# Performance work log

Hardware: AMD Instinct MI355X
Metric: run time of the kernel (lower is better)

The kernel has to match this reference:

```python
import jax, jax.numpy as jnp
import numpy as np

N = 50000   # nodes
E = 800000  # edges (before self-loops)
D = 256     # hidden_dim
H = 8       # heads
C = D // H  # 32 channels per head
NEG_SLOPE = 0.2


def setup_inputs() -> dict:
    key = jax.random.key(0)
    ks = jax.random.split(key, 10)
    sc = 0.05
    x = jax.random.normal(ks[0], (N, D), dtype=jnp.float32)
    edges_idx = jax.random.randint(ks[1], (2, E), 0, N, dtype=jnp.int64)
    # GATv2Conv params per layer: lin_l (W for source j), lin_r (W for target i), att [H,C], bias [H*C]
    Wl1 = jax.random.normal(ks[2], (D, H * C), dtype=jnp.float32) * sc
    Wr1 = jax.random.normal(ks[3], (D, H * C), dtype=jnp.float32) * sc
    att1 = jax.random.normal(ks[4], (H, C), dtype=jnp.float32) * sc
    b1 = jnp.zeros((H * C,), dtype=jnp.float32)
    Wl2 = jax.random.normal(ks[5], (D, H * C), dtype=jnp.float32) * sc
    Wr2 = jax.random.normal(ks[6], (D, H * C), dtype=jnp.float32) * sc
    att2 = jax.random.normal(ks[7], (H, C), dtype=jnp.float32) * sc
    b2 = jnp.zeros((H * C,), dtype=jnp.float32)
    return dict(x=x, edges_idx=edges_idx, Wl1=Wl1, Wr1=Wr1, att1=att1, b1=b1,
                Wl2=Wl2, Wr2=Wr2, att2=att2, b2=b2)


def gatv2_layer(x, src, dst, Wl, Wr, att, b):
    # x: [N, D]; src/dst: [E'] (self-loops included)
    xl = (x @ Wl).reshape(-1, H, C)  # source-side transform
    xr = (x @ Wr).reshape(-1, H, C)  # target-side transform
    # GATv2 score: e_ij = a^T LeakyReLU(Wl x_j + Wr x_i)
    z = jax.nn.leaky_relu(xl[src] + xr[dst], NEG_SLOPE)   # [E', H, C]
    e = jnp.einsum('ehc,hc->eh', z, att)                  # [E', H]
    # softmax over edges sharing the same target node (segment softmax)
    m = jax.ops.segment_max(e, dst, num_segments=N)       # [N, H]
    ex = jnp.exp(e - m[dst])
    s = jax.ops.segment_sum(ex, dst, num_segments=N)      # [N, H]
    alpha = ex / s[dst]                                   # [E', H]
    out = jax.ops.segment_sum(alpha[..., None] * xl[src], dst, num_segments=N)  # [N, H, C]
    return out.reshape(-1, H * C) + b


def reference(x, edges_idx, Wl1, Wr1, att1, b1, Wl2, Wr2, att2, b2):
    # PyG default add_self_loops=True
    loop = jnp.arange(N, dtype=edges_idx.dtype)
    src = jnp.concatenate([edges_idx[0], loop])
    dst = jnp.concatenate([edges_idx[1], loop])
    # layer 1 -> ELU -> layer 2 (dropout identity in eval mode)
    h = jax.nn.elu(gatv2_layer(x, src, dst, Wl1, Wr1, att1, b1))
    return gatv2_layer(h, src, dst, Wl2, Wr2, att2, b2)
```

## Files before the change

### kernel.cpp

```cpp
#include <hip/hip_runtime.h>
#include <hip/hip_bf16.h>
#include <math.h>

#define HEADS 8
#define HC 256
#define NEG_SLOPE 0.2f

typedef __attribute__((ext_vector_type(8))) short short8;
typedef __attribute__((ext_vector_type(16))) float floatx16;

__device__ inline ushort bf16_rne(float f) {
    unsigned u = __float_as_uint(f);
    return (ushort)((u + 0x7FFFu + ((u >> 16) & 1u)) >> 16);
}
__device__ inline float bf2f(ushort u) {
    return __uint_as_float(((unsigned)u) << 16);
}

__global__ __launch_bounds__(256) void cvt_bf16_sw(
        const float* __restrict__ x, ushort* __restrict__ xb, long long nblk) {
    long long id = (long long)blockIdx.x * blockDim.x + threadIdx.x;
    if (id >= nblk) return;
    long long r = id >> 5;
    int j = (int)(id & 31);
    const float4* p = (const float4*)(x + id * 8);
    float4 a = p[0], b = p[1];
    short8 pk;
    pk[0] = (short)bf16_rne(a.x); pk[1] = (short)bf16_rne(a.y);
    pk[2] = (short)bf16_rne(a.z); pk[3] = (short)bf16_rne(a.w);
    pk[4] = (short)bf16_rne(b.x); pk[5] = (short)bf16_rne(b.y);
    pk[6] = (short)bf16_rne(b.z); pk[7] = (short)bf16_rne(b.w);
    int jx = j ^ ((int)r & 7);
    *(short8*)(xb + r * 256 + jx * 8) = pk;
}

__global__ __launch_bounds__(256) void build_wt(
        const float* __restrict__ Wl, const float* __restrict__ Wr,
        ushort* __restrict__ wt) {
    int n = blockIdx.x;
    int k = threadIdx.x;
    const float* W = (n < 256) ? Wl : Wr;
    int col = n & 255;
    int jx = (k >> 3) ^ (n & 7);
    wt[n * HC + jx * 8 + (k & 7)] = bf16_rne(W[k * HC + col]);
}

__global__ __launch_bounds__(256) void gemm_mfma(
        const ushort* __restrict__ A, const ushort* __restrict__ wt,
        ushort* __restrict__ xl, ushort* __restrict__ xr, int N) {
    __shared__ ushort lA[64 * 256];
    __shared__ ushort lB[64 * 256];
    int local = blockIdx.x & 127;
    int grp   = blockIdx.x >> 7;
    int mt = grp * 16 + (local & 15);
    int nt = local >> 4;
    int m0 = mt * 64, n0 = nt * 64;
    int t = threadIdx.x;
    int lane = t & 63, wv = t >> 6;

    {
        const ushort* gA = A + (long long)m0 * HC;
        const ushort* gB = wt + (long long)n0 * HC;
        #pragma unroll
        for (int i = 0; i < 8; ++i) {
            int off = (wv * 8 + i) * 512;
            __builtin_amdgcn_global_load_lds(
                (const __attribute__((address_space(1))) unsigned int*)(gA + off + lane * 8),
                (__attribute__((address_space(3))) unsigned int*)(lA + off), 16, 0, 0);
            __builtin_amdgcn_global_load_lds(
                (const __attribute__((address_space(1))) unsigned int*)(gB + off + lane * 8),
                (__attribute__((address_space(3))) unsigned int*)(lB + off), 16, 0, 0);
        }
    }
    __syncthreads();

    int rA = (wv & 1) * 32 + (lane & 31);
    int rB = (wv >> 1) * 32 + (lane & 31);
    int kh = lane >> 5;
    int sA = rA & 7, sB = rB & 7;
    floatx16 acc;
    #pragma unroll
    for (int i = 0; i < 16; ++i) acc[i] = 0.f;
    #pragma unroll
    for (int step = 0; step < 16; ++step) {
        int j = step * 2 + kh;
        short8 a = *(const short8*)&lA[rA * 256 + ((j ^ sA) * 8)];
        short8 b = *(const short8*)&lB[rB * 256 + ((j ^ sB) * 8)];
        acc = __builtin_amdgcn_mfma_f32_32x32x16_bf16(a, b, acc, 0, 0, 0);
    }

    ushort* obase = (nt < 4) ? xl : xr;
    int colb = (n0 & 255) + (wv >> 1) * 32 + (lane & 31);
    int rbase = m0 + (wv & 1) * 32 + 4 * kh;
    #pragma unroll
    for (int g = 0; g < 4; ++g) {
        #pragma unroll
        for (int q = 0; q < 4; ++q) {
            int row = rbase + q + 8 * g;
            if (row < N)
                obase[(long long)row * HC + colb] = bf16_rne(acc[g * 4 + q]);
        }
    }
}

__global__ void hist_dst(const int* __restrict__ eidx, int E, int N,
                         int* __restrict__ counts) {
    int w = blockIdx.x * blockDim.x + threadIdx.x;
    int Etot = E + N;
    if (w >= Etot) return;
    int d = (w < E) ? eidx[E + w] : (w - E);
    atomicAdd(&counts[d], 1);
}

__global__ __launch_bounds__(1024) void scan_local(
        const int* __restrict__ counts, int* __restrict__ rowptr,
        int* __restrict__ bsum, int N) {
    __shared__ int wsums[16];
    int t = threadIdx.x, lane = t & 63, wv = t >> 6;
    int i = blockIdx.x * 1024 + t;
    int v = (i < N) ? counts[i] : 0;
    int orig = v;
    #pragma unroll
    for (int off = 1; off < 64; off <<= 1) {
        int n = __shfl_up(v, off, 64);
        if (lane >= off) v += n;
    }
    if (lane == 63) wsums[wv] = v;
    __syncthreads();
    int woff = 0, total = 0;
    #pragma unroll
    for (int w_ = 0; w_ < 16; ++w_) {
        int s = wsums[w_];
        if (w_ < wv) woff += s;
        total += s;
    }
    if (i < N) rowptr[i] = v + woff - orig;
    if (t == 0) bsum[blockIdx.x] = total;
}

__global__ void scan_bsums(const int* __restrict__ bsum, int* __restrict__ bsum2,
                           int* __restrict__ rowptr, int nb, int N) {
    int lane = threadIdx.x;
    int v = (lane < nb) ? bsum[lane] : 0;
    int orig = v;
    #pragma unroll
    for (int off = 1; off < 64; off <<= 1) {
        int n = __shfl_up(v, off, 64);
        if (lane >= off) v += n;
    }
    if (lane < nb) bsum2[lane] = v - orig;
    if (lane == 63) rowptr[N] = v;
}

__global__ __launch_bounds__(1024) void scan_add(
        int* __restrict__ rowptr, const int* __restrict__ bsum2, int N) {
    int i = blockIdx.x * 1024 + threadIdx.x;
    if (i < N) rowptr[i] += bsum2[blockIdx.x];
}

__global__ void scatter_edges(const int* __restrict__ eidx, int E, int N,
                              const int* __restrict__ rowptr,
                              int* __restrict__ fill, int* __restrict__ srcS) {
    int w = blockIdx.x * blockDim.x + threadIdx.x;
    int Etot = E + N;
    if (w >= Etot) return;
    int s, d;
    if (w < E) { s = eidx[w]; d = eidx[E + w]; }
    else       { s = w - E;   d = w - E; }
    int pos = rowptr[d] + atomicAdd(&fill[d], 1);
    srcS[pos] = s;
}

template <int LAYER1>
__global__ __launch_bounds__(256) void gat_node(
        const ushort* __restrict__ xl, const ushort* __restrict__ xr,
        const float* __restrict__ att, const float* __restrict__ bias,
        const int* __restrict__ rowptr, const int* __restrict__ srcS,
        void* __restrict__ outp, int N) {
    int node = blockIdx.x * 4 + (threadIdx.x >> 6);
    int lane = threadIdx.x & 63;
    if (node >= N) return;
    int beg = rowptr[node], end = rowptr[node + 1];

    ushort4 xu = *(const ushort4*)(xr + (long long)node * HC + lane * 4);
    float xr0 = bf2f(xu.x), xr1 = bf2f(xu.y), xr2 = bf2f(xu.z), xr3 = bf2f(xu.w);
    float4 atv = *(const float4*)(att + lane * 4);

    float ssA = 0.f, ssB = 0.f;
    float4 aA = make_float4(0.f, 0.f, 0.f, 0.f);
    float4 aB = make_float4(0.f, 0.f, 0.f, 0.f);

#define EDGE_BODY(P, SS, AC)                                                   \
    {                                                                          \
        int s = srcS[P];                                                       \
        ushort4 u = *(const ushort4*)(xl + (long long)s * HC + lane * 4);      \
        float v0 = bf2f(u.x), v1 = bf2f(u.y), v2 = bf2f(u.z), v3 = bf2f(u.w);  \
        float t0 = v0 + xr0, t1 = v1 + xr1, t2 = v2 + xr2, t3 = v3 + xr3;      \
        float st = atv.x * t0;                                                 \
        st = fmaf(atv.y, t1, st);                                              \
        st = fmaf(atv.z, t2, st);                                              \
        st = fmaf(atv.w, t3, st);                                              \
        float sa = atv.x * fabsf(t0);                                          \
        sa = fmaf(atv.y, fabsf(t1), sa);                                       \
        sa = fmaf(atv.z, fabsf(t2), sa);                                       \
        sa = fmaf(atv.w, fabsf(t3), sa);                                       \
        float sc = fmaf(0.6f, st, 0.4f * sa);                                  \
        sc += __shfl_xor(sc, 1, 64);                                           \
        sc += __shfl_xor(sc, 2, 64);                                           \
        sc += __shfl_xor(sc, 4, 64);                                           \
        float ex = __expf(sc);                                                 \
        SS += ex;                                                              \
        AC.x = fmaf(ex, v0, AC.x); AC.y = fmaf(ex, v1, AC.y);                  \
        AC.z = fmaf(ex, v2, AC.z); AC.w = fmaf(ex, v3, AC.w);                  \
    }

    int p = beg;
    for (; p + 1 < end; p += 2) {
        EDGE_BODY(p, ssA, aA)
        EDGE_BODY(p + 1, ssB, aB)
    }
    if (p < end) EDGE_BODY(p, ssA, aA)
#undef EDGE_BODY

    float inv = 1.f / (ssA + ssB);
    float4 bv = *(const float4*)(bias + lane * 4);
    float o0 = (aA.x + aB.x) * inv + bv.x;
    float o1 = (aA.y + aB.y) * inv + bv.y;
    float o2 = (aA.z + aB.z) * inv + bv.z;
    float o3 = (aA.w + aB.w) * inv + bv.w;
    if (LAYER1) {
        o0 = o0 > 0.f ? o0 : expm1f(o0);
        o1 = o1 > 0.f ? o1 : expm1f(o1);
        o2 = o2 > 0.f ? o2 : expm1f(o2);
        o3 = o3 > 0.f ? o3 : expm1f(o3);
        ushort4 pk;
        pk.x = bf16_rne(o0); pk.y = bf16_rne(o1);
        pk.z = bf16_rne(o2); pk.w = bf16_rne(o3);
        int jx = (lane >> 1) ^ (node & 7);
        *(ushort4*)((ushort*)outp + (long long)node * HC + jx * 8 +
                    (lane & 1) * 4) = pk;
    } else {
        *(float4*)((float*)outp + (long long)node * HC + lane * 4) =
            make_float4(o0, o1, o2, o3);
    }
}

extern "C" void kernel_launch(void* const* d_in, const int* in_sizes, int n_in,
                              void* d_out, int out_size, void* d_ws, size_t ws_size,
                              hipStream_t stream) {
    const float* x    = (const float*)d_in[0];
    const int*   eidx = (const int*)d_in[1];
    const float* Wl1  = (const float*)d_in[2];
    const float* Wr1  = (const float*)d_in[3];
    const float* att1 = (const float*)d_in[4];
    const float* b1   = (const float*)d_in[5];
    const float* Wl2  = (const float*)d_in[6];
    const float* Wr2  = (const float*)d_in[7];
    const float* att2 = (const float*)d_in[8];
    const float* b2   = (const float*)d_in[9];
    float* out = (float*)d_out;

    const int N = in_sizes[0] / HC;
    const int E = in_sizes[1] / 2;
    const int Etot = E + N;
    const long long NHC = (long long)N * HC;

    ushort* xl   = (ushort*)d_ws;
    ushort* xr   = xl + NHC;
    ushort* hbuf = xr + NHC;
    ushort* xb   = hbuf + NHC;
    ushort* wt1  = xb + NHC;
    ushort* wt2  = wt1 + 512 * HC;
    int* rowptr  = (int*)(wt2 + 512 * HC);
    int* counts  = rowptr + (N + 1);
    int* fill    = counts + N;
    int* bsum    = fill + N;
    int* bsum2   = bsum + 64;
    int* srcS    = bsum2 + 64;

    const int TB = 256;
    dim3 blk(TB);
    int gEdgesT = (Etot + TB - 1) / TB;
    int mtTiles = (N + 63) / 64;
    int gGemm   = ((mtTiles + 15) / 16) * 128;
    int gNode   = (N + 3) / 4;
    int nb      = (N + 1023) / 1024;
    long long nblk = NHC / 8;
    int gCvt    = (int)((nblk + TB - 1) / TB);

    cvt_bf16_sw<<<gCvt, blk, 0, stream>>>(x, xb, nblk);
    build_wt<<<512, blk, 0, stream>>>(Wl1, Wr1, wt1);
    build_wt<<<512, blk, 0, stream>>>(Wl2, Wr2, wt2);
    hipMemsetAsync(counts, 0, (size_t)2 * N * sizeof(int), stream);
    hist_dst<<<gEdgesT, blk, 0, stream>>>(eidx, E, N, counts);
    scan_local<<<nb, 1024, 0, stream>>>(counts, rowptr, bsum, N);
    scan_bsums<<<1, 64, 0, stream>>>(bsum, bsum2, rowptr, nb, N);
    scan_add<<<nb, 1024, 0, stream>>>(rowptr, bsum2, N);
    scatter_edges<<<gEdgesT, blk, 0, stream>>>(eidx, E, N, rowptr, fill, srcS);

    gemm_mfma<<<gGemm, blk, 0, stream>>>(xb, wt1, xl, xr, N);
    gat_node<1><<<gNode, blk, 0, stream>>>(xl, xr, att1, b1, rowptr, srcS, hbuf, N);

    gemm_mfma<<<gGemm, blk, 0, stream>>>(hbuf, wt2, xl, xr, N);
    gat_node<0><<<gNode, blk, 0, stream>>>(xl, xr, att2, b2, rowptr, srcS, out, N);
}
```

Baseline: 433.3 us.

## Split wavefront into two half-waves each processing a different edge with 16B loads

The node aggregation kernel now has each lane handle 8 channels with 16-byte loads. The two 32-lane halves of a wavefront process two different edges at once, and their partial sums and accumulators are combined with a cross-half shuffle at the end. The goal is to double edge-level parallelism per wave and widen gather loads, which should cut the per-edge instruction and latency overhead. In exchange it doubles the accumulator registers, adds masking for odd edge counts, and adds reduction shuffles plus select logic in the epilogue.

```diff
diff --git a/kernel.cpp b/kernel.cpp
--- a/kernel.cpp
+++ b/kernel.cpp
@@ -180,68 +180,120 @@
     int node = blockIdx.x * 4 + (threadIdx.x >> 6);
     int lane = threadIdx.x & 63;
     if (node >= N) return;
+    int h = lane >> 5;
+    unsigned coff = (unsigned)(lane & 31) * 8u;
     int beg = rowptr[node], end = rowptr[node + 1];
 
-    ushort4 xu = *(const ushort4*)(xr + (long long)node * HC + lane * 4);
-    float xr0 = bf2f(xu.x), xr1 = bf2f(xu.y), xr2 = bf2f(xu.z), xr3 = bf2f(xu.w);
-    float4 atv = *(const float4*)(att + lane * 4);
+    long long nbase = (long long)node * HC;
+    uint4 xu = *(const uint4*)(xr + nbase + coff);
+    float xr0 = __uint_as_float(xu.x << 16);
+    float xr1 = __uint_as_float(xu.x & 0xffff0000u);
+    float xr2 = __uint_as_float(xu.y << 16);
+    float xr3 = __uint_as_float(xu.y & 0xffff0000u);
+    float xr4 = __uint_as_float(xu.z << 16);
+    float xr5 = __uint_as_float(xu.z & 0xffff0000u);
+    float xr6 = __uint_as_float(xu.w << 16);
+    float xr7 = __uint_as_float(xu.w & 0xffff0000u);
+    float4 av0 = *(const float4*)(att + coff);
+    float4 av1 = *(const float4*)(att + coff + 4);
 
     float ssA = 0.f, ssB = 0.f;
-    float4 aA = make_float4(0.f, 0.f, 0.f, 0.f);
-    float4 aB = make_float4(0.f, 0.f, 0.f, 0.f);
-
-#define EDGE_BODY(P, SS, AC)                                                   \
+    float aA0 = 0.f, aA1 = 0.f, aA2 = 0.f, aA3 = 0.f;
+    float aA4 = 0.f, aA5 = 0.f, aA6 = 0.f, aA7 = 0.f;
+    float aB0 = 0.f, aB1 = 0.f, aB2 = 0.f, aB3 = 0.f;
+    float aB4 = 0.f, aB5 = 0.f, aB6 = 0.f, aB7 = 0.f;
+
+#define EDGE2(P, SFX, ALLV)                                                    \
     {                                                                          \
-        int s = srcS[P];                                                       \
-        ushort4 u = *(const ushort4*)(xl + (long long)s * HC + lane * 4);      \
-        float v0 = bf2f(u.x), v1 = bf2f(u.y), v2 = bf2f(u.z), v3 = bf2f(u.w);  \
+        int pe = (P) + ((ALLV) ? h : 0);                                       \
+        int s = srcS[pe];                                                      \
+        unsigned off = ((unsigned)s << 8) | coff;                              \
+        uint4 dv = *(const uint4*)(xl + off);                                  \
+        float v0 = __uint_as_float(dv.x << 16);                                \
+        float v1 = __uint_as_float(dv.x & 0xffff0000u);                        \
+        float v2 = __uint_as_float(dv.y << 16);                                \
+        float v3 = __uint_as_float(dv.y & 0xffff0000u);                        \
+        float v4 = __uint_as_float(dv.z << 16);                                \
+        float v5 = __uint_as_float(dv.z & 0xffff0000u);                        \
+        float v6 = __uint_as_float(dv.w << 16);                                \
+        float v7 = __uint_as_float(dv.w & 0xffff0000u);                        \
         float t0 = v0 + xr0, t1 = v1 + xr1, t2 = v2 + xr2, t3 = v3 + xr3;      \
-        float st = atv.x * t0;                                                 \
-        st = fmaf(atv.y, t1, st);                                              \
-        st = fmaf(atv.z, t2, st);                                              \
-        st = fmaf(atv.w, t3, st);                                              \
-        float sa = atv.x * fabsf(t0);                                          \
-        sa = fmaf(atv.y, fabsf(t1), sa);                                       \
-        sa = fmaf(atv.z, fabsf(t2), sa);                                       \
-        sa = fmaf(atv.w, fabsf(t3), sa);                                       \
+        float t4 = v4 + xr4, t5 = v5 + xr5, t6 = v6 + xr6, t7 = v7 + xr7;      \
+        float st = av0.x * t0;                                                 \
+        st = fmaf(av0.y, t1, st); st = fmaf(av0.z, t2, st);                    \
+        st = fmaf(av0.w, t3, st); st = fmaf(av1.x, t4, st);                    \
+        st = fmaf(av1.y, t5, st); st = fmaf(av1.z, t6, st);                    \
+        st = fmaf(av1.w, t7, st);                                              \
+        float sa = av0.x * fabsf(t0);                                          \
+        sa = fmaf(av0.y, fabsf(t1), sa); sa = fmaf(av0.z, fabsf(t2), sa);      \
+        sa = fmaf(av0.w, fabsf(t3), sa); sa = fmaf(av1.x, fabsf(t4), sa);      \
+        sa = fmaf(av1.y, fabsf(t5), sa); sa = fmaf(av1.z, fabsf(t6), sa);      \
+        sa = fmaf(av1.w, fabsf(t7), sa);                                       \
         float sc = fmaf(0.6f, st, 0.4f * sa);                                  \
         sc += __shfl_xor(sc, 1, 64);                                           \
         sc += __shfl_xor(sc, 2, 64);                                           \
-        sc += __shfl_xor(sc, 4, 64);                                           \
-        float ex = __expf(sc);                                                 \
-        SS += ex;                                                              \
-        AC.x = fmaf(ex, v0, AC.x); AC.y = fmaf(ex, v1, AC.y);                  \
-        AC.z = fmaf(ex, v2, AC.z); AC.w = fmaf(ex, v3, AC.w);                  \
+        float ex = ((ALLV) || h == 0) ? __expf(sc) : 0.f;                      \
+        ss##SFX += ex;                                                         \
+        a##SFX##0 = fmaf(ex, v0, a##SFX##0);                                   \
+        a##SFX##1 = fmaf(ex, v1, a##SFX##1);                                   \
+        a##SFX##2 = fmaf(ex, v2, a##SFX##2);                                   \
+        a##SFX##3 = fmaf(ex, v3, a##SFX##3);                                   \
+        a##SFX##4 = fmaf(ex, v4, a##SFX##4);                                   \
+        a##SFX##5 = fmaf(ex, v5, a##SFX##5);                                   \
+        a##SFX##6 = fmaf(ex, v6, a##SFX##6);                                   \
+        a##SFX##7 = fmaf(ex, v7, a##SFX##7);                                   \
     }
 
     int p = beg;
-    for (; p + 1 < end; p += 2) {
-        EDGE_BODY(p, ssA, aA)
-        EDGE_BODY(p + 1, ssB, aB)
-    }
-    if (p < end) EDGE_BODY(p, ssA, aA)
-#undef EDGE_BODY
-
-    float inv = 1.f / (ssA + ssB);
-    float4 bv = *(const float4*)(bias + lane * 4);
-    float o0 = (aA.x + aB.x) * inv + bv.x;
-    float o1 = (aA.y + aB.y) * inv + bv.y;
-    float o2 = (aA.z + aB.z) * inv + bv.z;
-    float o3 = (aA.w + aB.w) * inv + bv.w;
+    for (; p + 4 <= end; p += 4) {
+        EDGE2(p, A, 1)
+        EDGE2(p + 2, B, 1)
+    }
+    if (p + 2 <= end) { EDGE2(p, A, 1) p += 2; }
+    if (p < end) { EDGE2(p, B, 0) }
+#undef EDGE2
+
+    float ss = ssA + ssB;
+    ss += __shfl_xor(ss, 32, 64);
+    float a0 = aA0 + aB0; a0 += __shfl_xor(a0, 32, 64);
+    float a1 = aA1 + aB1; a1 += __shfl_xor(a1, 32, 64);
+    float a2 = aA2 + aB2; a2 += __shfl_xor(a2, 32, 64);
+    float a3 = aA3 + aB3; a3 += __shfl_xor(a3, 32, 64);
+    float a4 = aA4 + aB4; a4 += __shfl_xor(a4, 32, 64);
+    float a5 = aA5 + aB5; a5 += __shfl_xor(a5, 32, 64);
+    float a6 = aA6 + aB6; a6 += __shfl_xor(a6, 32, 64);
+    float a7 = aA7 + aB7; a7 += __shfl_xor(a7, 32, 64);
+
+    float inv = 1.f / ss;
+    float4 bv0 = *(const float4*)(bias + coff);
+    float4 bv1 = *(const float4*)(bias + coff + 4);
+    float o0 = fmaf(a0, inv, bv0.x);
+    float o1 = fmaf(a1, inv, bv0.y);
+    float o2 = fmaf(a2, inv, bv0.z);
+    float o3 = fmaf(a3, inv, bv0.w);
+    float o4 = fmaf(a4, inv, bv1.x);
+    float o5 = fmaf(a5, inv, bv1.y);
+    float o6 = fmaf(a6, inv, bv1.z);
+    float o7 = fmaf(a7, inv, bv1.w);
+
     if (LAYER1) {
-        o0 = o0 > 0.f ? o0 : expm1f(o0);
-        o1 = o1 > 0.f ? o1 : expm1f(o1);
-        o2 = o2 > 0.f ? o2 : expm1f(o2);
-        o3 = o3 > 0.f ? o3 : expm1f(o3);
+        float s0 = h ? o4 : o0;
+        float s1 = h ? o5 : o1;
+        float s2 = h ? o6 : o2;
+        float s3 = h ? o7 : o3;
+        s0 = s0 > 0.f ? s0 : expm1f(s0);
+        s1 = s1 > 0.f ? s1 : expm1f(s1);
+        s2 = s2 > 0.f ? s2 : expm1f(s2);
+        s3 = s3 > 0.f ? s3 : expm1f(s3);
         ushort4 pk;
-        pk.x = bf16_rne(o0); pk.y = bf16_rne(o1);
-        pk.z = bf16_rne(o2); pk.w = bf16_rne(o3);
-        int jx = (lane >> 1) ^ (node & 7);
-        *(ushort4*)((ushort*)outp + (long long)node * HC + jx * 8 +
-                    (lane & 1) * 4) = pk;
+        pk.x = bf16_rne(s0); pk.y = bf16_rne(s1);
+        pk.z = bf16_rne(s2); pk.w = bf16_rne(s3);
+        int jx = (lane & 31) ^ (node & 7);
+        *(ushort4*)((ushort*)outp + nbase + jx * 8 + h * 4) = pk;
     } else {
-        *(float4*)((float*)outp + (long long)node * HC + lane * 4) =
-            make_float4(o0, o1, o2, o3);
+        float4 ov = h ? make_float4(o4, o5, o6, o7)
+                      : make_float4(o0, o1, o2, o3);
+        *(float4*)((float*)outp + nbase + coff + h * 4) = ov;
     }
 }
 
```

Measured after the change: 412.6 us. 4.8% less time.

## Split wavefront into two edge streams with 16-byte gathers and packed math

Applied to the files above, without the earlier changes.

The aggregation kernel now splits each 64-lane wavefront into two halves, each half handling alternate edges. Each lane loads 16 bytes (8 bf16 values) per edge instead of 8, and the next edge's gather is software-prefetched. Source indices are pre-shifted into byte offsets, and the score math uses packed 2-wide floats with a DPP quad reduction. It also accumulates ex*(xl+xr) and subtracts xr at the end, and pads srcS with zeros so over-reads past the last edge stay safe. The aim is to cut gather latency and instruction count per edge, at the cost of a cross-half shuffle reduction and an index format tied to HC=256.

```diff
diff --git a/kernel.cpp b/kernel.cpp
--- a/kernel.cpp
+++ b/kernel.cpp
@@ -8,13 +8,26 @@
 
 typedef __attribute__((ext_vector_type(8))) short short8;
 typedef __attribute__((ext_vector_type(16))) float floatx16;
+typedef __attribute__((ext_vector_type(2))) float v2f;
 
 __device__ inline ushort bf16_rne(float f) {
     unsigned u = __float_as_uint(f);
     return (ushort)((u + 0x7FFFu + ((u >> 16) & 1u)) >> 16);
 }
-__device__ inline float bf2f(ushort u) {
-    return __uint_as_float(((unsigned)u) << 16);
+
+__device__ __forceinline__ v2f unpk2(unsigned u) {
+    v2f r;
+    r.x = __uint_as_float(u << 16);
+    r.y = __uint_as_float(u & 0xffff0000u);
+    return r;
+}
+
+__device__ __forceinline__ float quad_add(float x) {
+    x += __int_as_float(__builtin_amdgcn_mov_dpp(
+        __float_as_int(x), 0xB1, 0xF, 0xF, true));
+    x += __int_as_float(__builtin_amdgcn_mov_dpp(
+        __float_as_int(x), 0x4E, 0xF, 0xF, true));
+    return x;
 }
 
 __global__ __launch_bounds__(256) void cvt_bf16_sw(
@@ -168,80 +181,110 @@
     if (w < E) { s = eidx[w]; d = eidx[E + w]; }
     else       { s = w - E;   d = w - E; }
     int pos = rowptr[d] + atomicAdd(&fill[d], 1);
-    srcS[pos] = s;
+    srcS[pos] = s << 9;
 }
 
 template <int LAYER1>
 __global__ __launch_bounds__(256) void gat_node(
         const ushort* __restrict__ xl, const ushort* __restrict__ xr,
         const float* __restrict__ att, const float* __restrict__ bias,
-        const int* __restrict__ rowptr, const int* __restrict__ srcS,
+        const int* __restrict__ rowptr, const unsigned* __restrict__ srcB,
         void* __restrict__ outp, int N) {
     int node = blockIdx.x * 4 + (threadIdx.x >> 6);
     int lane = threadIdx.x & 63;
     if (node >= N) return;
+    int h = lane >> 5;
+    int q = lane & 31;
+    unsigned cb = (unsigned)q * 16u;
     int beg = rowptr[node], end = rowptr[node + 1];
-
-    ushort4 xu = *(const ushort4*)(xr + (long long)node * HC + lane * 4);
-    float xr0 = bf2f(xu.x), xr1 = bf2f(xu.y), xr2 = bf2f(xu.z), xr3 = bf2f(xu.w);
-    float4 atv = *(const float4*)(att + lane * 4);
-
-    float ssA = 0.f, ssB = 0.f;
-    float4 aA = make_float4(0.f, 0.f, 0.f, 0.f);
-    float4 aB = make_float4(0.f, 0.f, 0.f, 0.f);
-
-#define EDGE_BODY(P, SS, AC)                                                   \
-    {                                                                          \
-        int s = srcS[P];                                                       \
-        ushort4 u = *(const ushort4*)(xl + (long long)s * HC + lane * 4);      \
-        float v0 = bf2f(u.x), v1 = bf2f(u.y), v2 = bf2f(u.z), v3 = bf2f(u.w);  \
-        float t0 = v0 + xr0, t1 = v1 + xr1, t2 = v2 + xr2, t3 = v3 + xr3;      \
-        float st = atv.x * t0;                                                 \
-        st = fmaf(atv.y, t1, st);                                              \
-        st = fmaf(atv.z, t2, st);                                              \
-        st = fmaf(atv.w, t3, st);                                              \
-        float sa = atv.x * fabsf(t0);                                          \
-        sa = fmaf(atv.y, fabsf(t1), sa);                                       \
-        sa = fmaf(atv.z, fabsf(t2), sa);                                       \
-        sa = fmaf(atv.w, fabsf(t3), sa);                                       \
-        float sc = fmaf(0.6f, st, 0.4f * sa);                                  \
-        sc += __shfl_xor(sc, 1, 64);                                           \
-        sc += __shfl_xor(sc, 2, 64);                                           \
-        sc += __shfl_xor(sc, 4, 64);                                           \
-        float ex = __expf(sc);                                                 \
-        SS += ex;                                                              \
-        AC.x = fmaf(ex, v0, AC.x); AC.y = fmaf(ex, v1, AC.y);                  \
-        AC.z = fmaf(ex, v2, AC.z); AC.w = fmaf(ex, v3, AC.w);                  \
-    }
-
-    int p = beg;
-    for (; p + 1 < end; p += 2) {
-        EDGE_BODY(p, ssA, aA)
-        EDGE_BODY(p + 1, ssB, aB)
-    }
-    if (p < end) EDGE_BODY(p, ssA, aA)
-#undef EDGE_BODY
-
-    float inv = 1.f / (ssA + ssB);
-    float4 bv = *(const float4*)(bias + lane * 4);
-    float o0 = (aA.x + aB.x) * inv + bv.x;
-    float o1 = (aA.y + aB.y) * inv + bv.y;
-    float o2 = (aA.z + aB.z) * inv + bv.z;
-    float o3 = (aA.w + aB.w) * inv + bv.w;
+    int np = (end - beg + 1) >> 1;
+
+    long long nbase = (long long)node * HC;
+    uint4 xu = *(const uint4*)(xr + nbase + q * 8);
+    v2f X0 = unpk2(xu.x), X1 = unpk2(xu.y), X2 = unpk2(xu.z), X3 = unpk2(xu.w);
+    v2f A0 = *(const v2f*)(att + q * 8);
+    v2f A1 = *(const v2f*)(att + q * 8 + 2);
+    v2f A2 = *(const v2f*)(att + q * 8 + 4);
+    v2f A3 = *(const v2f*)(att + q * 8 + 6);
+
+    float ss = 0.f;
+    v2f C0 = {0.f, 0.f}, C1 = {0.f, 0.f}, C2 = {0.f, 0.f}, C3 = {0.f, 0.f};
+
+    const char* xb = (const char*)xl;
+    int eP = beg + h;
+    unsigned offN = srcB[eP + 2];
+    uint4 dv = *(const uint4*)(xb + (srcB[eP] | cb));
+
+    for (int i = 0; i < np; ++i) {
+        unsigned offN2 = srcB[eP + 4];
+        uint4 dvN = *(const uint4*)(xb + (offN | cb));
+        v2f t0 = unpk2(dv.x) + X0;
+        v2f t1 = unpk2(dv.y) + X1;
+        v2f t2 = unpk2(dv.z) + X2;
+        v2f t3 = unpk2(dv.w) + X3;
+        v2f m0 = t0 * NEG_SLOPE, m1 = t1 * NEG_SLOPE;
+        v2f m2 = t2 * NEG_SLOPE, m3 = t3 * NEG_SLOPE;
+        v2f l0, l1, l2, l3;
+        l0.x = fmaxf(t0.x, m0.x); l0.y = fmaxf(t0.y, m0.y);
+        l1.x = fmaxf(t1.x, m1.x); l1.y = fmaxf(t1.y, m1.y);
+        l2.x = fmaxf(t2.x, m2.x); l2.y = fmaxf(t2.y, m2.y);
+        l3.x = fmaxf(t3.x, m3.x); l3.y = fmaxf(t3.y, m3.y);
+        v2f d = A0 * l0;
+        d = __builtin_elementwise_fma(A1, l1, d);
+        d = __builtin_elementwise_fma(A2, l2, d);
+        d = __builtin_elementwise_fma(A3, l3, d);
+        float sc = quad_add(d.x + d.y);
+        float ex = __expf(sc);
+        ex = (eP < end) ? ex : 0.f;
+        ss += ex;
+        v2f e2 = {ex, ex};
+        C0 = __builtin_elementwise_fma(e2, t0, C0);
+        C1 = __builtin_elementwise_fma(e2, t1, C1);
+        C2 = __builtin_elementwise_fma(e2, t2, C2);
+        C3 = __builtin_elementwise_fma(e2, t3, C3);
+        offN = offN2; dv = dvN; eP += 2;
+    }
+
+    ss += __shfl_xor(ss, 32, 64);
+    float a0 = C0.x; a0 += __shfl_xor(a0, 32, 64);
+    float a1 = C0.y; a1 += __shfl_xor(a1, 32, 64);
+    float a2 = C1.x; a2 += __shfl_xor(a2, 32, 64);
+    float a3 = C1.y; a3 += __shfl_xor(a3, 32, 64);
+    float a4 = C2.x; a4 += __shfl_xor(a4, 32, 64);
+    float a5 = C2.y; a5 += __shfl_xor(a5, 32, 64);
+    float a6 = C3.x; a6 += __shfl_xor(a6, 32, 64);
+    float a7 = C3.y; a7 += __shfl_xor(a7, 32, 64);
+
+    float inv = 1.f / ss;
+    float4 bv0 = *(const float4*)(bias + q * 8);
+    float4 bv1 = *(const float4*)(bias + q * 8 + 4);
+    float o0 = fmaf(a0, inv, bv0.x - X0.x);
+    float o1 = fmaf(a1, inv, bv0.y - X0.y);
+    float o2 = fmaf(a2, inv, bv0.z - X1.x);
+    float o3 = fmaf(a3, inv, bv0.w - X1.y);
+    float o4 = fmaf(a4, inv, bv1.x - X2.x);
+    float o5 = fmaf(a5, inv, bv1.y - X2.y);
+    float o6 = fmaf(a6, inv, bv1.z - X3.x);
+    float o7 = fmaf(a7, inv, bv1.w - X3.y);
+
     if (LAYER1) {
-        o0 = o0 > 0.f ? o0 : expm1f(o0);
-        o1 = o1 > 0.f ? o1 : expm1f(o1);
-        o2 = o2 > 0.f ? o2 : expm1f(o2);
-        o3 = o3 > 0.f ? o3 : expm1f(o3);
+        float s0 = h ? o4 : o0;
+        float s1 = h ? o5 : o1;
+        float s2 = h ? o6 : o2;
+        float s3 = h ? o7 : o3;
+        s0 = s0 > 0.f ? s0 : expm1f(s0);
+        s1 = s1 > 0.f ? s1 : expm1f(s1);
+        s2 = s2 > 0.f ? s2 : expm1f(s2);
+        s3 = s3 > 0.f ? s3 : expm1f(s3);
         ushort4 pk;
-        pk.x = bf16_rne(o0); pk.y = bf16_rne(o1);
-        pk.z = bf16_rne(o2); pk.w = bf16_rne(o3);
-        int jx = (lane >> 1) ^ (node & 7);
-        *(ushort4*)((ushort*)outp + (long long)node * HC + jx * 8 +
-                    (lane & 1) * 4) = pk;
+        pk.x = bf16_rne(s0); pk.y = bf16_rne(s1);
+        pk.z = bf16_rne(s2); pk.w = bf16_rne(s3);
+        int jx = q ^ (node & 7);
+        *(ushort4*)((ushort*)outp + nbase + jx * 8 + h * 4) = pk;
     } else {
-        *(float4*)((float*)outp + (long long)node * HC + lane * 4) =
-            make_float4(o0, o1, o2, o3);
+        float4 ov = h ? make_float4(o4, o5, o6, o7)
+                      : make_float4(o0, o1, o2, o3);
+        *(float4*)((float*)outp + nbase + q * 8 + h * 4) = ov;
     }
 }
 
@@ -292,6 +335,7 @@
     build_wt<<<512, blk, 0, stream>>>(Wl1, Wr1, wt1);
     build_wt<<<512, blk, 0, stream>>>(Wl2, Wr2, wt2);
     hipMemsetAsync(counts, 0, (size_t)2 * N * sizeof(int), stream);
+    hipMemsetAsync(srcS + Etot, 0, 8 * sizeof(int), stream);
     hist_dst<<<gEdgesT, blk, 0, stream>>>(eidx, E, N, counts);
     scan_local<<<nb, 1024, 0, stream>>>(counts, rowptr, bsum, N);
     scan_bsums<<<1, 64, 0, stream>>>(bsum, bsum2, rowptr, nb, N);
@@ -299,8 +343,10 @@
     scatter_edges<<<gEdgesT, blk, 0, stream>>>(eidx, E, N, rowptr, fill, srcS);
 
     gemm_mfma<<<gGemm, blk, 0, stream>>>(xb, wt1, xl, xr, N);
-    gat_node<1><<<gNode, blk, 0, stream>>>(xl, xr, att1, b1, rowptr, srcS, hbuf, N);
+    gat_node<1><<<gNode, blk, 0, stream>>>(xl, xr, att1, b1, rowptr,
+                                           (const unsigned*)srcS, hbuf, N);
 
     gemm_mfma<<<gGemm, blk, 0, stream>>>(hbuf, wt2, xl, xr, N);
-    gat_node<0><<<gNode, blk, 0, stream>>>(xl, xr, att2, b2, rowptr, srcS, out, N);
-}
+    gat_node<0><<<gNode, blk, 0, stream>>>(xl, xr, att2, b2, rowptr,
+                                           (const unsigned*)srcS, out, N);
+}
```

Measured after the change: 432.5 us. Within noise of the previous version (-0.2%).
